# Kernel optimization log

Hardware: AMD Instinct MI355X
Metric: run time of the kernel (lower is better)

Reference implementation:

```python
import jax, jax.numpy as jnp
import numpy as np

C = 384      # c_s
NF = 16      # n_freq
H = 256      # mlp_hidden
B, K, N = 4, 2048, 16384
POS_WEIGHT = 1.5  # not used; see below


def _ln(x, g, b, eps=1e-5):
    m = x.mean(-1, keepdims=True)
    v = ((x - m) ** 2).mean(-1, keepdims=True)
    return (x - m) * jax.lax.rsqrt(v + eps) * g + b


def setup_inputs() -> dict:
    key = jax.random.key(0)
    ks = jax.random.split(key, 24)
    w = lambda k, shp: (jax.random.normal(k, shp, jnp.float32) * 0.02)
    inp = {
        "s_parent": jax.random.normal(ks[0], (B, K, C), jnp.float32),
        "mu_k": jax.random.normal(ks[1], (B, K, 3), jnp.float32),
        "R_k": jax.random.normal(ks[2], (B, K, 3, 3), jnp.float32),
        "s_k": jax.random.uniform(ks[3], (B, K, 3), jnp.float32),
        "a_idx": jax.random.randint(ks[4], (B, N), 0, K, jnp.int32),
        "node_mask": jnp.ones((B, N), jnp.float32),
        "pos01": jax.random.uniform(ks[5], (B, N), jnp.float32),
        # Pos01FourierEncoder: Linear(2*NF -> C)
        "pos_w": w(ks[6], (C, 2 * NF)), "pos_b": jnp.zeros((C,), jnp.float32),
        # q_proj: LayerNorm(C), Linear(C,C), SiLU, Linear(C,C)
        "q_ln_g": jnp.ones((C,), jnp.float32), "q_ln_b": jnp.zeros((C,), jnp.float32),
        "q_w1": w(ks[7], (C, C)), "q_b1": jnp.zeros((C,), jnp.float32),
        "q_w2": w(ks[8], (C, C)), "q_b2": jnp.zeros((C,), jnp.float32),
        # mlp: LayerNorm(C), Linear(C,H), SiLU, Linear(H,H), SiLU, Linear(H,3)
        "m_ln_g": jnp.ones((C,), jnp.float32), "m_ln_b": jnp.zeros((C,), jnp.float32),
        "m_w1": w(ks[9], (H, C)), "m_b1": jnp.zeros((H,), jnp.float32),
        "m_w2": w(ks[10], (H, H)), "m_b2": jnp.zeros((H,), jnp.float32),
        "m_w3": w(ks[11], (3, H)), "m_b3": jnp.zeros((3,), jnp.float32),
    }
    return inp


def reference(s_parent, mu_k, R_k, s_k, a_idx, node_mask, pos01,
              pos_w, pos_b, q_ln_g, q_ln_b, q_w1, q_b1, q_w2, q_b2,
              m_ln_g, m_ln_b, m_w1, m_b1, m_w2, m_b2, m_w3, m_b3):
    pos_weight = 1.0
    scale = 1.5
    mask = node_mask[..., None]  # [B,N,1]

    # Fourier positional encoding of pos01 in [0,1]
    freqs = (2.0 ** jnp.arange(NF, dtype=jnp.float32)) * np.float32(np.pi)
    ang = pos01[..., None] * freqs                          # [B,N,NF]
    feats = jnp.concatenate([jnp.sin(ang), jnp.cos(ang)], -1)  # [B,N,2NF]
    pos_emb = (feats @ pos_w.T + pos_b) * mask              # [B,N,C]

    idx = jnp.clip(a_idx, 0, K - 1)
    s_pi = jnp.take_along_axis(s_parent, idx[:, :, None], axis=1)  # [B,N,C]
    s_pi = s_pi + pos_weight * pos_emb

    # q_proj
    q = _ln(s_pi, q_ln_g, q_ln_b)
    q = jax.nn.silu(q @ q_w1.T + q_b1)
    q = (q @ q_w2.T + q_b2) * mask

    # mlp -> xi_hat
    h = _ln(q, m_ln_g, m_ln_b)
    h = jax.nn.silu(h @ m_w1.T + m_b1)
    h = jax.nn.silu(h @ m_w2.T + m_b2)
    xi = (h @ m_w3.T + m_b3) * mask
    xi_hat = jnp.tanh(xi) * scale                           # [B,N,3]

    # gather parent rigid params per node
    mu_i = jnp.take_along_axis(mu_k, idx[:, :, None], axis=1)            # [B,N,3]
    s_i = jnp.take_along_axis(jnp.maximum(s_k, 1e-8), idx[:, :, None], axis=1)
    R_i = jnp.take_along_axis(R_k, idx[:, :, None, None], axis=1)        # [B,N,3,3]

    # rigid apply: x = R @ (xi * s) + mu
    x_hat = jnp.einsum('bnij,bnj->bni', R_i, xi_hat * s_i) + mu_i
    x_hat = x_hat * mask
    return xi_hat, x_hat * 10.0, pos01
```

## Files before the change

### kernel.cpp

```cpp
#include <hip/hip_runtime.h>
#include <hip/hip_bf16.h>
#include <math.h>

#define C 384
#define NF 16
#define H 256
#define Bb 4
#define Kk 2048
#define Nn 16384
#define MB 32
#define LDA 392

typedef __attribute__((ext_vector_type(8))) short bf16x8;
typedef __attribute__((ext_vector_type(4))) float f32x4;
typedef __attribute__((ext_vector_type(4))) short s16x4;

#define POS_OFF 0
#define Q1_OFF  12288
#define Q2_OFF  159744
#define M1_OFF  307200
#define M2_OFF  405504
#define M3_OFF  471040
#define W_TOTAL 475136
#define NCONV   ((W_TOTAL + 255) / 256)
#define GQ_OFF 0
#define CQ_OFF 384
#define GM_OFF 768
#define CM_OFF 1024

__device__ __attribute__((always_inline)) inline short f2bf(float x) {
    return __builtin_bit_cast(short, __float2bfloat16(x));
}
__device__ __attribute__((always_inline)) inline float bf2f(short s) {
    return __bfloat162float(__builtin_bit_cast(__hip_bfloat16, s));
}
__device__ __attribute__((always_inline)) inline float silu(float v) {
    return v * __builtin_amdgcn_rcpf(1.f + __expf(-v));
}
__device__ __attribute__((always_inline)) inline s16x4 pack4(f32x4 v) {
    __hip_bfloat162 p0 = __float22bfloat162_rn(float2{v[0], v[1]});
    __hip_bfloat162 p1 = __float22bfloat162_rn(float2{v[2], v[3]});
    s16x4 o;
    o[0] = __builtin_bit_cast(short, p0.x);
    o[1] = __builtin_bit_cast(short, p0.y);
    o[2] = __builtin_bit_cast(short, p1.x);
    o[3] = __builtin_bit_cast(short, p1.y);
    return o;
}

__global__ __launch_bounds__(256) void prep(
    const float* __restrict__ pos_w, const float* __restrict__ q_w1,
    const float* __restrict__ q_w2,  const float* __restrict__ m_w1,
    const float* __restrict__ m_w2,  const float* __restrict__ m_w3,
    const float* __restrict__ q_ln_g, const float* __restrict__ q_ln_b,
    const float* __restrict__ m_ln_g, const float* __restrict__ m_ln_b,
    const float* __restrict__ q_b1,   const float* __restrict__ m_b1,
    short* __restrict__ ws, float* __restrict__ cst)
{
    __shared__ float rg[4], rc[4];
    int tid = threadIdx.x;
    int blk = blockIdx.x;
    if (blk < NCONV) {
        int i = blk * 256 + tid;
        if (i >= W_TOTAL) return;
        const float* src; int off, K;
        if      (i < Q1_OFF) { src = pos_w; off = POS_OFF; K = 32; }
        else if (i < Q2_OFF) { src = q_w1;  off = Q1_OFF;  K = 384; }
        else if (i < M1_OFF) { src = q_w2;  off = Q2_OFF;  K = 384; }
        else if (i < M2_OFF) { src = m_w1;  off = M1_OFF;  K = 384; }
        else if (i < M3_OFF) { src = m_w2;  off = M2_OFF;  K = 256; }
        else                 { src = m_w3;  off = M3_OFF;  K = 256; }
        int t = i - off;
        int chunk = t >> 9, r = t & 511;
        int ln = r >> 5, kq = r & 31;
        int NKm = K >> 5;
        int ntg = chunk / NKm, kk = chunk - ntg * NKm;
        int f = ntg * 16 + ln, k = kk * 32 + kq;
        float v;
        if (off == M3_OFF) v = (f < 3) ? m_w3[f * 256 + k] : 0.f;
        else               v = src[(size_t)f * K + k];
        if (off == Q1_OFF) v *= q_ln_g[k];
        if (off == M1_OFF) v *= m_ln_g[k];
        ws[i] = f2bf(v);
        return;
    }
    int f = blk - NCONV;
    const float *Wsrc, *lng, *lnb, *bias; int fr, go, co;
    if (f < 384) { Wsrc = q_w1; lng = q_ln_g; lnb = q_ln_b; bias = q_b1; fr = f;      go = GQ_OFF; co = CQ_OFF; }
    else         { Wsrc = m_w1; lng = m_ln_g; lnb = m_ln_b; bias = m_b1; fr = f - 384; go = GM_OFF; co = CM_OFF; }
    float g = 0.f, c = 0.f;
    for (int k = tid; k < 384; k += 256) {
        float wv = Wsrc[(size_t)fr * 384 + k];
        g += bf2f(f2bf(wv * lng[k]));
        c += wv * lnb[k];
    }
    #pragma unroll
    for (int d = 1; d < 64; d <<= 1) { g += __shfl_xor(g, d); c += __shfl_xor(c, d); }
    if ((tid & 63) == 0) { rg[tid >> 6] = g; rc[tid >> 6] = c; }
    __syncthreads();
    if (tid == 0) {
        cst[go + fr] = rg[0] + rg[1] + rg[2] + rg[3];
        cst[co + fr] = rc[0] + rc[1] + rc[2] + rc[3] + bias[fr];
    }
}

template<int K, int NT, int NTN, int KN, bool SILU_, bool MASK, bool LNIN, bool STATS>
__device__ __attribute__((always_inline)) inline void layer_ip(
    const short* __restrict__ W, const float* __restrict__ cb,
    const float* __restrict__ Gf, int FB,
    const short* __restrict__ Wn, int FBn,
    bf16x8 (&bin)[6],
    short (*__restrict__ xs)[LDA],
    float (*__restrict__ sc1)[4], float (*__restrict__ sc2)[4],
    const float* __restrict__ wmask, int w, int q, int ln)
{
    constexpr int NK = K / 32;
    const short* bp[NT];
    #pragma unroll
    for (int nt = 0; nt < NT; ++nt)
        bp[nt] = W + ((size_t)(FB / 16 + nt) * NK) * 512 + ln * 32 + q * 8;

    f32x4 acc[2][NT];
    #pragma unroll
    for (int mt = 0; mt < 2; ++mt)
        #pragma unroll
        for (int nt = 0; nt < NT; ++nt)
            acc[mt][nt] = (f32x4){0.f, 0.f, 0.f, 0.f};

    bf16x8 b0[NT], b1[NT], a0[2], a1[2];
    #pragma unroll
    for (int nt = 0; nt < NT; ++nt) b0[nt] = bin[nt];
    #pragma unroll
    for (int mt = 0; mt < 2; ++mt) a0[mt] = *(const bf16x8*)&xs[mt * 16 + ln][q * 8];

    #pragma unroll
    for (int kc = 0; kc < NK; kc += 2) {
        #pragma unroll
        for (int nt = 0; nt < NT; ++nt) b1[nt] = *(const bf16x8*)(bp[nt] + (kc + 1) * 512);
        #pragma unroll
        for (int mt = 0; mt < 2; ++mt) a1[mt] = *(const bf16x8*)&xs[mt * 16 + ln][(kc + 1) * 32 + q * 8];
        #pragma unroll
        for (int nt = 0; nt < NT; ++nt)
            #pragma unroll
            for (int mt = 0; mt < 2; ++mt)
                acc[mt][nt] = __builtin_amdgcn_mfma_f32_16x16x32_bf16(b0[nt], a0[mt], acc[mt][nt], 0, 0, 0);
        if (kc + 2 < NK) {
            #pragma unroll
            for (int nt = 0; nt < NT; ++nt) b0[nt] = *(const bf16x8*)(bp[nt] + (kc + 2) * 512);
            #pragma unroll
            for (int mt = 0; mt < 2; ++mt) a0[mt] = *(const bf16x8*)&xs[mt * 16 + ln][(kc + 2) * 32 + q * 8];
        }
        #pragma unroll
        for (int nt = 0; nt < NT; ++nt)
            #pragma unroll
            for (int mt = 0; mt < 2; ++mt)
                acc[mt][nt] = __builtin_amdgcn_mfma_f32_16x16x32_bf16(b1[nt], a1[mt], acc[mt][nt], 0, 0, 0);
    }

    #pragma unroll
    for (int nt = 0; nt < NTN; ++nt)
        bin[nt] = *(const bf16x8*)(Wn + ((size_t)(FBn / 16 + nt) * (KN / 32)) * 512 + ln * 32 + q * 8);

    __syncthreads();

    float mk[2], rstd[2], rm[2];
    #pragma unroll
    for (int mt = 0; mt < 2; ++mt) {
        int m = mt * 16 + ln;
        if (MASK) mk[mt] = wmask[m];
        if (LNIN) {
            f32x4 p1 = *(const f32x4*)&sc1[m][0];
            f32x4 p2 = *(const f32x4*)&sc2[m][0];
            float t1 = p1[0] + p1[1] + p1[2] + p1[3];
            float t2 = p2[0] + p2[1] + p2[2] + p2[3];
            float mean = t1 * (1.f / 384.f);
            float var  = t2 * (1.f / 384.f) - mean * mean;
            rstd[mt] = rsqrtf(var + 1e-5f);
            rm[mt]   = rstd[mt] * mean;
        }
    }

    float s1[2] = {0.f, 0.f}, s2[2] = {0.f, 0.f};
    #pragma unroll
    for (int nt = 0; nt < NT; ++nt) {
        const int f0 = FB + nt * 16 + q * 4;
        f32x4 c4 = *(const f32x4*)&cb[f0];
        f32x4 g4;
        if (LNIN) g4 = *(const f32x4*)&Gf[f0];
        #pragma unroll
        for (int mt = 0; mt < 2; ++mt) {
            f32x4 vv;
            #pragma unroll
            for (int r = 0; r < 4; ++r) {
                float v;
                if (LNIN) v = fmaf(rstd[mt], acc[mt][nt][r], fmaf(-rm[mt], g4[r], c4[r]));
                else      v = acc[mt][nt][r] + c4[r];
                if (SILU_) v = silu(v);
                if (MASK) v *= mk[mt];
                if (STATS) { s1[mt] += v; s2[mt] += v * v; }
                vv[r] = v;
            }
            *(s16x4*)&xs[mt * 16 + ln][f0] = pack4(vv);
        }
    }
    if (STATS) {
        #pragma unroll
        for (int mt = 0; mt < 2; ++mt) {
            s1[mt] += __shfl_xor(s1[mt], 16); s2[mt] += __shfl_xor(s2[mt], 16);
            s1[mt] += __shfl_xor(s1[mt], 32); s2[mt] += __shfl_xor(s2[mt], 32);
        }
        if (q == 0) {
            #pragma unroll
            for (int mt = 0; mt < 2; ++mt) {
                sc1[mt * 16 + ln][w] = s1[mt];
                sc2[mt * 16 + ln][w] = s2[mt];
            }
        }
    }
    __syncthreads();
}

__global__ __launch_bounds__(256, 3) void upxi32(
    const float* __restrict__ s_parent, const float* __restrict__ mu_k,
    const float* __restrict__ R_k,      const float* __restrict__ s_k,
    const int*   __restrict__ a_idx,    const float* __restrict__ node_mask,
    const float* __restrict__ pos01,
    const float* __restrict__ pos_b,
    const float* __restrict__ q_b2,     const float* __restrict__ m_b2,
    const float* __restrict__ m_b3,
    const short* __restrict__ wsb,      const float* __restrict__ cst,
    float* __restrict__ out)
{
    __shared__ short xs[MB][LDA];
    __shared__ float sc1[MB][4];
    __shared__ float sc2[MB][4];
    __shared__ float wmask[MB], wpos[MB];
    __shared__ int   widx[MB];

    const int tid  = threadIdx.x;
    const int w    = tid >> 6;
    const int lane = tid & 63;
    const int q    = lane >> 4;
    const int ln   = lane & 15;

    const int g0 = blockIdx.x * MB;
    const int b  = g0 / Nn;
    const int n0 = g0 % Nn;

    bf16x8 bin[6];
    #pragma unroll
    for (int nt = 0; nt < 6; ++nt)
        bin[nt] = *(const bf16x8*)(wsb + Q1_OFF + ((size_t)(w * 6 + nt) * 12) * 512 + ln * 32 + q * 8);

    if (tid < MB) {
        int gi = b * Nn + n0 + tid;
        int idx = a_idx[gi];
        widx[tid]  = min(max(idx, 0), Kk - 1);
        wmask[tid] = node_mask[gi];
        wpos[tid]  = pos01[gi];
    }
    __syncthreads();

    const float* gbase = s_parent + (long)b * Kk * C;

    {
        const short* pos_wb = wsb + POS_OFF;
        const bool use_sin = (q < 2);
        const int kb = (q & 1) * 8;
        bf16x8 a[2];
        #pragma unroll
        for (int mt = 0; mt < 2; ++mt) {
            float p = wpos[mt * 16 + ln];
            #pragma unroll
            for (int e = 0; e < 8; ++e) {
                float fr = (float)(1 << (kb + e)) * 3.14159265358979323846f;
                float sv, cv;
                __sincosf(p * fr, &sv, &cv);
                a[mt][e] = f2bf(use_sin ? sv : cv);
            }
        }
        f32x4 acc[2][6];
        #pragma unroll
        for (int mt = 0; mt < 2; ++mt)
            #pragma unroll
            for (int nt = 0; nt < 6; ++nt)
                acc[mt][nt] = (f32x4){0.f, 0.f, 0.f, 0.f};
        #pragma unroll
        for (int nt = 0; nt < 6; ++nt) {
            bf16x8 bfr = *(const bf16x8*)&pos_wb[(w * 6 + nt) * 512 + ln * 32 + q * 8];
            #pragma unroll
            for (int mt = 0; mt < 2; ++mt)
                acc[mt][nt] = __builtin_amdgcn_mfma_f32_16x16x32_bf16(bfr, a[mt], acc[mt][nt], 0, 0, 0);
        }
        float mk[2]; int ix[2];
        #pragma unroll
        for (int mt = 0; mt < 2; ++mt) {
            mk[mt] = wmask[mt * 16 + ln];
            ix[mt] = widx[mt * 16 + ln];
        }
        float s1[2] = {0.f, 0.f}, s2[2] = {0.f, 0.f};
        #pragma unroll
        for (int nt = 0; nt < 6; ++nt) {
            const int f0 = w * 96 + nt * 16 + q * 4;
            f32x4 pb4 = *(const f32x4*)&pos_b[f0];
            #pragma unroll
            for (int mt = 0; mt < 2; ++mt) {
                f32x4 g4 = *(const f32x4*)&gbase[(long)ix[mt] * C + f0];
                f32x4 vv;
                #pragma unroll
                for (int r = 0; r < 4; ++r) {
                    float v = (acc[mt][nt][r] + pb4[r]) * mk[mt] + g4[r];
                    s1[mt] += v; s2[mt] += v * v;
                    vv[r] = v;
                }
                *(s16x4*)&xs[mt * 16 + ln][f0] = pack4(vv);
            }
        }
        #pragma unroll
        for (int mt = 0; mt < 2; ++mt) {
            s1[mt] += __shfl_xor(s1[mt], 16); s2[mt] += __shfl_xor(s2[mt], 16);
            s1[mt] += __shfl_xor(s1[mt], 32); s2[mt] += __shfl_xor(s2[mt], 32);
        }
        if (q == 0) {
            #pragma unroll
            for (int mt = 0; mt < 2; ++mt) {
                sc1[mt * 16 + ln][w] = s1[mt];
                sc2[mt * 16 + ln][w] = s2[mt];
            }
        }
    }
    __syncthreads();

    layer_ip<384, 6, 6, 384, true,  false, true,  false>(wsb + Q1_OFF, cst + CQ_OFF,
        cst + GQ_OFF, w * 96, wsb + Q2_OFF, w * 96, bin, xs, sc1, sc2, wmask, w, q, ln);
    layer_ip<384, 6, 4, 384, false, true,  false, true >(wsb + Q2_OFF, q_b2,
        nullptr, w * 96, wsb + M1_OFF, w * 64, bin, xs, sc1, sc2, wmask, w, q, ln);
    layer_ip<384, 4, 4, 256, true,  false, true,  false>(wsb + M1_OFF, cst + CM_OFF,
        cst + GM_OFF, w * 64, wsb + M2_OFF, w * 64, bin, xs, sc1, sc2, wmask, w, q, ln);
    layer_ip<256, 4, 1, 256, true,  false, false, false>(wsb + M2_OFF, m_b2,
        nullptr, w * 64, wsb + M3_OFF, 0, bin, xs, sc1, sc2, wmask, w, q, ln);

    if (w < 2) {
        const short* W3 = wsb + M3_OFF;
        f32x4 a3 = (f32x4){0.f, 0.f, 0.f, 0.f};
        #pragma unroll
        for (int kc = 0; kc < 8; ++kc) {
            bf16x8 a  = *(const bf16x8*)&xs[w * 16 + ln][kc * 32 + q * 8];
            bf16x8 bf = *(const bf16x8*)(W3 + kc * 512 + ln * 32 + q * 8);
            a3 = __builtin_amdgcn_mfma_f32_16x16x32_bf16(bf, a, a3, 0, 0, 0);
        }
        if (q == 0) {
            int m = w * 16 + ln;
            float mkv = wmask[m];
            #pragma unroll
            for (int r = 0; r < 3; ++r) {
                float v = (a3[r] + m_b3[r]) * mkv;
                sc1[m][r] = tanhf(v) * 1.5f;
            }
        }
        if (lane < 16) {
            int m = w * 16 + lane;
            long gi = (long)b * Nn + n0 + m;
            long pk = (long)b * Kk + widx[m];
            float mkv = wmask[m];
            float xv[3], yv[3], xiv[3];
            #pragma unroll
            for (int j = 0; j < 3; ++j) {
                xiv[j] = sc1[m][j];
                float sc = fmaxf(s_k[pk * 3 + j], 1e-8f);
                xv[j] = xiv[j] * sc;
            }
            #pragma unroll
            for (int i = 0; i < 3; ++i) {
                float a = R_k[pk * 9 + i * 3 + 0] * xv[0]
                        + R_k[pk * 9 + i * 3 + 1] * xv[1]
                        + R_k[pk * 9 + i * 3 + 2] * xv[2]
                        + mu_k[pk * 3 + i];
                yv[i] = a * mkv * 10.f;
            }
            float* o0 = out;
            float* o1 = out + (long)Bb * Nn * 3;
            float* o2 = out + (long)Bb * Nn * 6;
            #pragma unroll
            for (int j = 0; j < 3; ++j) { o0[gi * 3 + j] = xiv[j]; o1[gi * 3 + j] = yv[j]; }
            o2[gi] = wpos[m];
        }
    }
}

extern "C" void kernel_launch(void* const* d_in, const int* in_sizes, int n_in,
                              void* d_out, int out_size, void* d_ws, size_t ws_size,
                              hipStream_t stream) {
    const float* s_parent = (const float*)d_in[0];
    const float* mu_k     = (const float*)d_in[1];
    const float* R_k      = (const float*)d_in[2];
    const float* s_k      = (const float*)d_in[3];
    const int*   a_idx    = (const int*)  d_in[4];
    const float* node_mask= (const float*)d_in[5];
    const float* pos01    = (const float*)d_in[6];
    const float* pos_w    = (const float*)d_in[7];
    const float* pos_b    = (const float*)d_in[8];
    const float* q_ln_g   = (const float*)d_in[9];
    const float* q_ln_b   = (const float*)d_in[10];
    const float* q_w1     = (const float*)d_in[11];
    const float* q_b1     = (const float*)d_in[12];
    const float* q_w2     = (const float*)d_in[13];
    const float* q_b2     = (const float*)d_in[14];
    const float* m_ln_g   = (const float*)d_in[15];
    const float* m_ln_b   = (const float*)d_in[16];
    const float* m_w1     = (const float*)d_in[17];
    const float* m_b1     = (const float*)d_in[18];
    const float* m_w2     = (const float*)d_in[19];
    const float* m_b2     = (const float*)d_in[20];
    const float* m_w3     = (const float*)d_in[21];
    const float* m_b3     = (const float*)d_in[22];

    short* wsb = (short*)d_ws;
    float* cst = (float*)(wsb + W_TOTAL);

    prep<<<NCONV + 640, 256, 0, stream>>>(
        pos_w, q_w1, q_w2, m_w1, m_w2, m_w3,
        q_ln_g, q_ln_b, m_ln_g, m_ln_b, q_b1, m_b1, wsb, cst);

    int blocks = (Bb * Nn) / MB;
    upxi32<<<blocks, 256, 0, stream>>>(
        s_parent, mu_k, R_k, s_k, a_idx, node_mask, pos01,
        pos_b, q_b2, m_b2, m_b3, wsb, cst, (float*)d_out);
}
```

Baseline: 236.1 us.

## Double the row tile to 64 and triple-buffer weight fragment loads

Each block now handles 64 rows instead of 32, so every weight fragment fetched from global memory feeds four MFMA row tiles instead of two, halving weight traffic per row. The K loop becomes a 3-stage rotating buffer for weight fragments with the next layer's first fragments prefetched inside the loop, and __syncthreads is replaced by a raw lgkmcnt wait plus barrier. The final 3-wide head now runs on all four waves. The cost is more accumulator registers and a drop in launch-bounds occupancy from 3 to 2 blocks per CU.

```diff
diff --git a/kernel.cpp b/kernel.cpp
--- a/kernel.cpp
+++ b/kernel.cpp
@@ -8,7 +8,7 @@
 #define Bb 4
 #define Kk 2048
 #define Nn 16384
-#define MB 32
+#define MB 64
 #define LDA 392
 
 typedef __attribute__((ext_vector_type(8))) short bf16x8;
@@ -27,6 +27,8 @@
 #define CQ_OFF 384
 #define GM_OFF 768
 #define CM_OFF 1024
+
+#define BAR() __asm__ volatile("s_waitcnt lgkmcnt(0)\ns_barrier" ::: "memory")
 
 __device__ __attribute__((always_inline)) inline short f2bf(float x) {
     return __builtin_bit_cast(short, __float2bfloat16(x));
@@ -115,57 +117,56 @@
     const float* __restrict__ wmask, int w, int q, int ln)
 {
     constexpr int NK = K / 32;
-    const short* bp[NT];
-    #pragma unroll
-    for (int nt = 0; nt < NT; ++nt)
-        bp[nt] = W + ((size_t)(FB / 16 + nt) * NK) * 512 + ln * 32 + q * 8;
-
-    f32x4 acc[2][NT];
-    #pragma unroll
-    for (int mt = 0; mt < 2; ++mt)
+    const short* bp = W + (size_t)(FB / 16) * NK * 512 + ln * 32 + q * 8;
+
+    f32x4 acc[4][NT];
+    #pragma unroll
+    for (int mt = 0; mt < 4; ++mt)
         #pragma unroll
         for (int nt = 0; nt < NT; ++nt)
             acc[mt][nt] = (f32x4){0.f, 0.f, 0.f, 0.f};
 
-    bf16x8 b0[NT], b1[NT], a0[2], a1[2];
-    #pragma unroll
-    for (int nt = 0; nt < NT; ++nt) b0[nt] = bin[nt];
-    #pragma unroll
-    for (int mt = 0; mt < 2; ++mt) a0[mt] = *(const bf16x8*)&xs[mt * 16 + ln][q * 8];
-
-    #pragma unroll
-    for (int kc = 0; kc < NK; kc += 2) {
-        #pragma unroll
-        for (int nt = 0; nt < NT; ++nt) b1[nt] = *(const bf16x8*)(bp[nt] + (kc + 1) * 512);
-        #pragma unroll
-        for (int mt = 0; mt < 2; ++mt) a1[mt] = *(const bf16x8*)&xs[mt * 16 + ln][(kc + 1) * 32 + q * 8];
+    bf16x8 Bbuf[3][NT], Abuf[2][4];
+    #pragma unroll
+    for (int nt = 0; nt < NT; ++nt) Bbuf[0][nt] = bin[nt];
+    #pragma unroll
+    for (int nt = 0; nt < NT; ++nt)
+        Bbuf[1][nt] = *(const bf16x8*)(bp + (size_t)nt * NK * 512 + 512);
+    #pragma unroll
+    for (int mt = 0; mt < 4; ++mt)
+        Abuf[0][mt] = *(const bf16x8*)&xs[mt * 16 + ln][q * 8];
+
+    #pragma unroll
+    for (int kc = 0; kc < NK; ++kc) {
+        if (kc + 2 < NK) {
+            #pragma unroll
+            for (int nt = 0; nt < NT; ++nt)
+                Bbuf[(kc + 2) % 3][nt] =
+                    *(const bf16x8*)(bp + (size_t)nt * NK * 512 + (kc + 2) * 512);
+        } else if (kc + 2 == NK) {
+            #pragma unroll
+            for (int nt = 0; nt < NTN; ++nt)
+                bin[nt] = *(const bf16x8*)(Wn + ((size_t)(FBn / 16 + nt) * (KN / 32)) * 512 + ln * 32 + q * 8);
+        }
+        if (kc + 1 < NK) {
+            #pragma unroll
+            for (int mt = 0; mt < 4; ++mt)
+                Abuf[(kc + 1) & 1][mt] =
+                    *(const bf16x8*)&xs[mt * 16 + ln][(kc + 1) * 32 + q * 8];
+        }
         #pragma unroll
         for (int nt = 0; nt < NT; ++nt)
             #pragma unroll
-            for (int mt = 0; mt < 2; ++mt)
-                acc[mt][nt] = __builtin_amdgcn_mfma_f32_16x16x32_bf16(b0[nt], a0[mt], acc[mt][nt], 0, 0, 0);
-        if (kc + 2 < NK) {
-            #pragma unroll
-            for (int nt = 0; nt < NT; ++nt) b0[nt] = *(const bf16x8*)(bp[nt] + (kc + 2) * 512);
-            #pragma unroll
-            for (int mt = 0; mt < 2; ++mt) a0[mt] = *(const bf16x8*)&xs[mt * 16 + ln][(kc + 2) * 32 + q * 8];
-        }
-        #pragma unroll
-        for (int nt = 0; nt < NT; ++nt)
-            #pragma unroll
-            for (int mt = 0; mt < 2; ++mt)
-                acc[mt][nt] = __builtin_amdgcn_mfma_f32_16x16x32_bf16(b1[nt], a1[mt], acc[mt][nt], 0, 0, 0);
-    }
-
-    #pragma unroll
-    for (int nt = 0; nt < NTN; ++nt)
-        bin[nt] = *(const bf16x8*)(Wn + ((size_t)(FBn / 16 + nt) * (KN / 32)) * 512 + ln * 32 + q * 8);
-
-    __syncthreads();
-
-    float mk[2], rstd[2], rm[2];
-    #pragma unroll
-    for (int mt = 0; mt < 2; ++mt) {
+            for (int mt = 0; mt < 4; ++mt)
+                acc[mt][nt] = __builtin_amdgcn_mfma_f32_16x16x32_bf16(
+                    Bbuf[kc % 3][nt], Abuf[kc & 1][mt], acc[mt][nt], 0, 0, 0);
+    }
+
+    BAR();
+
+    float mk[4], rstd[4], rm[4];
+    #pragma unroll
+    for (int mt = 0; mt < 4; ++mt) {
         int m = mt * 16 + ln;
         if (MASK) mk[mt] = wmask[m];
         if (LNIN) {
@@ -180,7 +181,7 @@
         }
     }
 
-    float s1[2] = {0.f, 0.f}, s2[2] = {0.f, 0.f};
+    float s1[4] = {0.f,0.f,0.f,0.f}, s2[4] = {0.f,0.f,0.f,0.f};
     #pragma unroll
     for (int nt = 0; nt < NT; ++nt) {
         const int f0 = FB + nt * 16 + q * 4;
@@ -188,7 +189,7 @@
         f32x4 g4;
         if (LNIN) g4 = *(const f32x4*)&Gf[f0];
         #pragma unroll
-        for (int mt = 0; mt < 2; ++mt) {
+        for (int mt = 0; mt < 4; ++mt) {
             f32x4 vv;
             #pragma unroll
             for (int r = 0; r < 4; ++r) {
@@ -205,22 +206,22 @@
     }
     if (STATS) {
         #pragma unroll
-        for (int mt = 0; mt < 2; ++mt) {
+        for (int mt = 0; mt < 4; ++mt) {
             s1[mt] += __shfl_xor(s1[mt], 16); s2[mt] += __shfl_xor(s2[mt], 16);
             s1[mt] += __shfl_xor(s1[mt], 32); s2[mt] += __shfl_xor(s2[mt], 32);
         }
         if (q == 0) {
             #pragma unroll
-            for (int mt = 0; mt < 2; ++mt) {
+            for (int mt = 0; mt < 4; ++mt) {
                 sc1[mt * 16 + ln][w] = s1[mt];
                 sc2[mt * 16 + ln][w] = s2[mt];
             }
         }
     }
-    __syncthreads();
-}
-
-__global__ __launch_bounds__(256, 3) void upxi32(
+    BAR();
+}
+
+__global__ __launch_bounds__(256, 2) void upxi64(
     const float* __restrict__ s_parent, const float* __restrict__ mu_k,
     const float* __restrict__ R_k,      const float* __restrict__ s_k,
     const int*   __restrict__ a_idx,    const float* __restrict__ node_mask,
@@ -259,7 +260,7 @@
         wmask[tid] = node_mask[gi];
         wpos[tid]  = pos01[gi];
     }
-    __syncthreads();
+    BAR();
 
     const float* gbase = s_parent + (long)b * Kk * C;
 
@@ -267,9 +268,9 @@
         const short* pos_wb = wsb + POS_OFF;
         const bool use_sin = (q < 2);
         const int kb = (q & 1) * 8;
-        bf16x8 a[2];
-        #pragma unroll
-        for (int mt = 0; mt < 2; ++mt) {
+        bf16x8 a[4];
+        #pragma unroll
+        for (int mt = 0; mt < 4; ++mt) {
             float p = wpos[mt * 16 + ln];
             #pragma unroll
             for (int e = 0; e < 8; ++e) {
@@ -279,9 +280,9 @@
                 a[mt][e] = f2bf(use_sin ? sv : cv);
             }
         }
-        f32x4 acc[2][6];
-        #pragma unroll
-        for (int mt = 0; mt < 2; ++mt)
+        f32x4 acc[4][6];
+        #pragma unroll
+        for (int mt = 0; mt < 4; ++mt)
             #pragma unroll
             for (int nt = 0; nt < 6; ++nt)
                 acc[mt][nt] = (f32x4){0.f, 0.f, 0.f, 0.f};
@@ -289,22 +290,22 @@
         for (int nt = 0; nt < 6; ++nt) {
             bf16x8 bfr = *(const bf16x8*)&pos_wb[(w * 6 + nt) * 512 + ln * 32 + q * 8];
             #pragma unroll
-            for (int mt = 0; mt < 2; ++mt)
+            for (int mt = 0; mt < 4; ++mt)
                 acc[mt][nt] = __builtin_amdgcn_mfma_f32_16x16x32_bf16(bfr, a[mt], acc[mt][nt], 0, 0, 0);
         }
-        float mk[2]; int ix[2];
-        #pragma unroll
-        for (int mt = 0; mt < 2; ++mt) {
+        float mk[4]; int ix[4];
+        #pragma unroll
+        for (int mt = 0; mt < 4; ++mt) {
             mk[mt] = wmask[mt * 16 + ln];
             ix[mt] = widx[mt * 16 + ln];
         }
-        float s1[2] = {0.f, 0.f}, s2[2] = {0.f, 0.f};
+        float s1[4] = {0.f,0.f,0.f,0.f}, s2[4] = {0.f,0.f,0.f,0.f};
         #pragma unroll
         for (int nt = 0; nt < 6; ++nt) {
             const int f0 = w * 96 + nt * 16 + q * 4;
             f32x4 pb4 = *(const f32x4*)&pos_b[f0];
             #pragma unroll
-            for (int mt = 0; mt < 2; ++mt) {
+            for (int mt = 0; mt < 4; ++mt) {
                 f32x4 g4 = *(const f32x4*)&gbase[(long)ix[mt] * C + f0];
                 f32x4 vv;
                 #pragma unroll
@@ -317,19 +318,19 @@
             }
         }
         #pragma unroll
-        for (int mt = 0; mt < 2; ++mt) {
+        for (int mt = 0; mt < 4; ++mt) {
             s1[mt] += __shfl_xor(s1[mt], 16); s2[mt] += __shfl_xor(s2[mt], 16);
             s1[mt] += __shfl_xor(s1[mt], 32); s2[mt] += __shfl_xor(s2[mt], 32);
         }
         if (q == 0) {
             #pragma unroll
-            for (int mt = 0; mt < 2; ++mt) {
+            for (int mt = 0; mt < 4; ++mt) {
                 sc1[mt * 16 + ln][w] = s1[mt];
                 sc2[mt * 16 + ln][w] = s2[mt];
             }
         }
     }
-    __syncthreads();
+    BAR();
 
     layer_ip<384, 6, 6, 384, true,  false, true,  false>(wsb + Q1_OFF, cst + CQ_OFF,
         cst + GQ_OFF, w * 96, wsb + Q2_OFF, w * 96, bin, xs, sc1, sc2, wmask, w, q, ln);
@@ -340,13 +341,14 @@
     layer_ip<256, 4, 1, 256, true,  false, false, false>(wsb + M2_OFF, m_b2,
         nullptr, w * 64, wsb + M3_OFF, 0, bin, xs, sc1, sc2, wmask, w, q, ln);
 
-    if (w < 2) {
+    {
         const short* W3 = wsb + M3_OFF;
         f32x4 a3 = (f32x4){0.f, 0.f, 0.f, 0.f};
         #pragma unroll
         for (int kc = 0; kc < 8; ++kc) {
             bf16x8 a  = *(const bf16x8*)&xs[w * 16 + ln][kc * 32 + q * 8];
-            bf16x8 bf = *(const bf16x8*)(W3 + kc * 512 + ln * 32 + q * 8);
+            bf16x8 bf = (kc == 0) ? bin[0]
+                      : *(const bf16x8*)(W3 + kc * 512 + ln * 32 + q * 8);
             a3 = __builtin_amdgcn_mfma_f32_16x16x32_bf16(bf, a, a3, 0, 0, 0);
         }
         if (q == 0) {
@@ -358,33 +360,34 @@
                 sc1[m][r] = tanhf(v) * 1.5f;
             }
         }
-        if (lane < 16) {
-            int m = w * 16 + lane;
-            long gi = (long)b * Nn + n0 + m;
-            long pk = (long)b * Kk + widx[m];
-            float mkv = wmask[m];
-            float xv[3], yv[3], xiv[3];
-            #pragma unroll
-            for (int j = 0; j < 3; ++j) {
-                xiv[j] = sc1[m][j];
-                float sc = fmaxf(s_k[pk * 3 + j], 1e-8f);
-                xv[j] = xiv[j] * sc;
-            }
-            #pragma unroll
-            for (int i = 0; i < 3; ++i) {
-                float a = R_k[pk * 9 + i * 3 + 0] * xv[0]
-                        + R_k[pk * 9 + i * 3 + 1] * xv[1]
-                        + R_k[pk * 9 + i * 3 + 2] * xv[2]
-                        + mu_k[pk * 3 + i];
-                yv[i] = a * mkv * 10.f;
-            }
-            float* o0 = out;
-            float* o1 = out + (long)Bb * Nn * 3;
-            float* o2 = out + (long)Bb * Nn * 6;
-            #pragma unroll
-            for (int j = 0; j < 3; ++j) { o0[gi * 3 + j] = xiv[j]; o1[gi * 3 + j] = yv[j]; }
-            o2[gi] = wpos[m];
-        }
+    }
+
+    if (lane < 16) {
+        int m = w * 16 + lane;
+        long gi = (long)b * Nn + n0 + m;
+        long pk = (long)b * Kk + widx[m];
+        float mkv = wmask[m];
+        float xv[3], yv[3], xiv[3];
+        #pragma unroll
+        for (int j = 0; j < 3; ++j) {
+            xiv[j] = sc1[m][j];
+            float sc = fmaxf(s_k[pk * 3 + j], 1e-8f);
+            xv[j] = xiv[j] * sc;
+        }
+        #pragma unroll
+        for (int i = 0; i < 3; ++i) {
+            float a = R_k[pk * 9 + i * 3 + 0] * xv[0]
+                    + R_k[pk * 9 + i * 3 + 1] * xv[1]
+                    + R_k[pk * 9 + i * 3 + 2] * xv[2]
+                    + mu_k[pk * 3 + i];
+            yv[i] = a * mkv * 10.f;
+        }
+        float* o0 = out;
+        float* o1 = out + (long)Bb * Nn * 3;
+        float* o2 = out + (long)Bb * Nn * 6;
+        #pragma unroll
+        for (int j = 0; j < 3; ++j) { o0[gi * 3 + j] = xiv[j]; o1[gi * 3 + j] = yv[j]; }
+        o2[gi] = wpos[m];
     }
 }
 
@@ -423,7 +426,7 @@
         q_ln_g, q_ln_b, m_ln_g, m_ln_b, q_b1, m_b1, wsb, cst);
 
     int blocks = (Bb * Nn) / MB;
-    upxi32<<<blocks, 256, 0, stream>>>(
+    upxi64<<<blocks, 256, 0, stream>>>(
         s_parent, mu_k, R_k, s_k, a_idx, node_mask, pos01,
         pos_b, q_b2, m_b2, m_b3, wsb, cst, (float*)d_out);
 }
```

After: 197.3 us. -16.4%, faster.

## Switch MLP chain to 32x32x16 MFMA with 64-row tiles and deeper weight prefetch

Applied to the files above, without the earlier changes.

Moves all GEMM layers from 16x16x32 to 32x32x16 bf16 MFMA, doubles rows per block to 64, and repacks the preprocessed weight layout to match the new fragment shape. The weight stream gets a 4-deep register ring buffer, and __syncthreads is replaced by a raw lgkmcnt wait plus s_barrier. The intent is to halve per-row weight traffic from L2 and raise MFMA efficiency, at the cost of more accumulator registers and lower occupancy (launch bounds 3 to 2).

```diff
diff --git a/kernel.cpp b/kernel.cpp
--- a/kernel.cpp
+++ b/kernel.cpp
@@ -8,12 +8,13 @@
 #define Bb 4
 #define Kk 2048
 #define Nn 16384
-#define MB 32
+#define MB 64
 #define LDA 392
 
-typedef __attribute__((ext_vector_type(8))) short bf16x8;
-typedef __attribute__((ext_vector_type(4))) float f32x4;
-typedef __attribute__((ext_vector_type(4))) short s16x4;
+typedef __attribute__((ext_vector_type(8)))  short bf16x8;
+typedef __attribute__((ext_vector_type(4)))  float f32x4;
+typedef __attribute__((ext_vector_type(16))) float f32x16;
+typedef __attribute__((ext_vector_type(4)))  short s16x4;
 
 #define POS_OFF 0
 #define Q1_OFF  12288
@@ -21,12 +22,14 @@
 #define M1_OFF  307200
 #define M2_OFF  405504
 #define M3_OFF  471040
-#define W_TOTAL 475136
+#define W_TOTAL 479232
 #define NCONV   ((W_TOTAL + 255) / 256)
 #define GQ_OFF 0
 #define CQ_OFF 384
 #define GM_OFF 768
 #define CM_OFF 1024
+
+#define BAR() __asm__ volatile("s_waitcnt lgkmcnt(0)\ns_barrier" ::: "memory")
 
 __device__ __attribute__((always_inline)) inline short f2bf(float x) {
     return __builtin_bit_cast(short, __float2bfloat16(x));
@@ -72,10 +75,11 @@
         else                 { src = m_w3;  off = M3_OFF;  K = 256; }
         int t = i - off;
         int chunk = t >> 9, r = t & 511;
-        int ln = r >> 5, kq = r & 31;
-        int NKm = K >> 5;
+        int lane = r >> 3, j = r & 7;
+        int lnn = lane & 31, half = lane >> 5;
+        int NKm = K >> 4;
         int ntg = chunk / NKm, kk = chunk - ntg * NKm;
-        int f = ntg * 16 + ln, k = kk * 32 + kq;
+        int f = ntg * 32 + lnn, k = kk * 16 + half * 8 + j;
         float v;
         if (off == M3_OFF) v = (f < 3) ? m_w3[f * 256 + k] : 0.f;
         else               v = src[(size_t)f * K + k];
@@ -109,64 +113,68 @@
     const short* __restrict__ W, const float* __restrict__ cb,
     const float* __restrict__ Gf, int FB,
     const short* __restrict__ Wn, int FBn,
-    bf16x8 (&bin)[6],
+    bf16x8 (&bin)[3],
     short (*__restrict__ xs)[LDA],
     float (*__restrict__ sc1)[4], float (*__restrict__ sc2)[4],
-    const float* __restrict__ wmask, int w, int q, int ln)
+    const float* __restrict__ wmask, int w, int lane)
 {
-    constexpr int NK = K / 32;
+    constexpr int NK = K / 16;
+    const int ln = lane & 31, half = lane >> 5;
     const short* bp[NT];
     #pragma unroll
     for (int nt = 0; nt < NT; ++nt)
-        bp[nt] = W + ((size_t)(FB / 16 + nt) * NK) * 512 + ln * 32 + q * 8;
-
-    f32x4 acc[2][NT];
+        bp[nt] = W + (size_t)(FB / 32 + nt) * NK * 512 + lane * 8;
+
+    f32x16 acc[2][NT];
     #pragma unroll
     for (int mt = 0; mt < 2; ++mt)
         #pragma unroll
         for (int nt = 0; nt < NT; ++nt)
-            acc[mt][nt] = (f32x4){0.f, 0.f, 0.f, 0.f};
-
-    bf16x8 b0[NT], b1[NT], a0[2], a1[2];
-    #pragma unroll
-    for (int nt = 0; nt < NT; ++nt) b0[nt] = bin[nt];
-    #pragma unroll
-    for (int mt = 0; mt < 2; ++mt) a0[mt] = *(const bf16x8*)&xs[mt * 16 + ln][q * 8];
-
-    #pragma unroll
-    for (int kc = 0; kc < NK; kc += 2) {
-        #pragma unroll
-        for (int nt = 0; nt < NT; ++nt) b1[nt] = *(const bf16x8*)(bp[nt] + (kc + 1) * 512);
-        #pragma unroll
-        for (int mt = 0; mt < 2; ++mt) a1[mt] = *(const bf16x8*)&xs[mt * 16 + ln][(kc + 1) * 32 + q * 8];
+            acc[mt][nt] = (f32x16)(0.f);
+
+    bf16x8 B[4][NT], a0[2], a1[2];
+    #pragma unroll
+    for (int nt = 0; nt < NT; ++nt) B[0][nt] = bin[nt];
+    #pragma unroll
+    for (int nt = 0; nt < NT; ++nt) B[1][nt] = *(const bf16x8*)(bp[nt] + 512);
+    #pragma unroll
+    for (int nt = 0; nt < NT; ++nt) B[2][nt] = *(const bf16x8*)(bp[nt] + 1024);
+    #pragma unroll
+    for (int mt = 0; mt < 2; ++mt)
+        a0[mt] = *(const bf16x8*)&xs[mt * 32 + ln][half * 8];
+
+    #pragma unroll
+    for (int kc = 0; kc < NK; ++kc) {
+        if (kc + 3 < NK) {
+            #pragma unroll
+            for (int nt = 0; nt < NT; ++nt)
+                B[(kc + 3) & 3][nt] = *(const bf16x8*)(bp[nt] + (kc + 3) * 512);
+        } else if (kc + 3 == NK) {
+            #pragma unroll
+            for (int nt = 0; nt < NTN; ++nt)
+                bin[nt] = *(const bf16x8*)(Wn + (size_t)(FBn / 32 + nt) * (KN / 16) * 512 + lane * 8);
+        }
+        bf16x8* ac = (kc & 1) ? a1 : a0;
+        bf16x8* an = (kc & 1) ? a0 : a1;
+        if (kc + 1 < NK) {
+            #pragma unroll
+            for (int mt = 0; mt < 2; ++mt)
+                an[mt] = *(const bf16x8*)&xs[mt * 32 + ln][(kc + 1) * 16 + half * 8];
+        }
         #pragma unroll
         for (int nt = 0; nt < NT; ++nt)
             #pragma unroll
             for (int mt = 0; mt < 2; ++mt)
-                acc[mt][nt] = __builtin_amdgcn_mfma_f32_16x16x32_bf16(b0[nt], a0[mt], acc[mt][nt], 0, 0, 0);
-        if (kc + 2 < NK) {
-            #pragma unroll
-            for (int nt = 0; nt < NT; ++nt) b0[nt] = *(const bf16x8*)(bp[nt] + (kc + 2) * 512);
-            #pragma unroll
-            for (int mt = 0; mt < 2; ++mt) a0[mt] = *(const bf16x8*)&xs[mt * 16 + ln][(kc + 2) * 32 + q * 8];
-        }
-        #pragma unroll
-        for (int nt = 0; nt < NT; ++nt)
-            #pragma unroll
-            for (int mt = 0; mt < 2; ++mt)
-                acc[mt][nt] = __builtin_amdgcn_mfma_f32_16x16x32_bf16(b1[nt], a1[mt], acc[mt][nt], 0, 0, 0);
-    }
-
-    #pragma unroll
-    for (int nt = 0; nt < NTN; ++nt)
-        bin[nt] = *(const bf16x8*)(Wn + ((size_t)(FBn / 16 + nt) * (KN / 32)) * 512 + ln * 32 + q * 8);
-
-    __syncthreads();
+                acc[mt][nt] = __builtin_amdgcn_mfma_f32_32x32x16_bf16(
+                    B[kc & 3][nt], ac[mt], acc[mt][nt], 0, 0, 0);
+    }
+
+    BAR();
 
     float mk[2], rstd[2], rm[2];
     #pragma unroll
     for (int mt = 0; mt < 2; ++mt) {
-        int m = mt * 16 + ln;
+        int m = mt * 32 + ln;
         if (MASK) mk[mt] = wmask[m];
         if (LNIN) {
             f32x4 p1 = *(const f32x4*)&sc1[m][0];
@@ -183,44 +191,48 @@
     float s1[2] = {0.f, 0.f}, s2[2] = {0.f, 0.f};
     #pragma unroll
     for (int nt = 0; nt < NT; ++nt) {
-        const int f0 = FB + nt * 16 + q * 4;
-        f32x4 c4 = *(const f32x4*)&cb[f0];
-        f32x4 g4;
-        if (LNIN) g4 = *(const f32x4*)&Gf[f0];
+        #pragma unroll
+        for (int g = 0; g < 4; ++g) {
+            const int f0 = FB + nt * 32 + 8 * g + 4 * half;
+            f32x4 c4 = *(const f32x4*)&cb[f0];
+            f32x4 g4;
+            if (LNIN) g4 = *(const f32x4*)&Gf[f0];
+            #pragma unroll
+            for (int mt = 0; mt < 2; ++mt) {
+                f32x4 vv;
+                #pragma unroll
+                for (int i = 0; i < 4; ++i) {
+                    float av = acc[mt][nt][4 * g + i];
+                    float v;
+                    if (LNIN) v = fmaf(rstd[mt], av, fmaf(-rm[mt], g4[i], c4[i]));
+                    else      v = av + c4[i];
+                    if (SILU_) v = silu(v);
+                    if (MASK) v *= mk[mt];
+                    if (STATS) { s1[mt] += v; s2[mt] += v * v; }
+                    vv[i] = v;
+                }
+                *(s16x4*)&xs[mt * 32 + ln][f0] = pack4(vv);
+            }
+        }
+    }
+    if (STATS) {
         #pragma unroll
         for (int mt = 0; mt < 2; ++mt) {
-            f32x4 vv;
-            #pragma unroll
-            for (int r = 0; r < 4; ++r) {
-                float v;
-                if (LNIN) v = fmaf(rstd[mt], acc[mt][nt][r], fmaf(-rm[mt], g4[r], c4[r]));
-                else      v = acc[mt][nt][r] + c4[r];
-                if (SILU_) v = silu(v);
-                if (MASK) v *= mk[mt];
-                if (STATS) { s1[mt] += v; s2[mt] += v * v; }
-                vv[r] = v;
-            }
-            *(s16x4*)&xs[mt * 16 + ln][f0] = pack4(vv);
-        }
-    }
-    if (STATS) {
-        #pragma unroll
-        for (int mt = 0; mt < 2; ++mt) {
-            s1[mt] += __shfl_xor(s1[mt], 16); s2[mt] += __shfl_xor(s2[mt], 16);
-            s1[mt] += __shfl_xor(s1[mt], 32); s2[mt] += __shfl_xor(s2[mt], 32);
-        }
-        if (q == 0) {
+            s1[mt] += __shfl_xor(s1[mt], 32);
+            s2[mt] += __shfl_xor(s2[mt], 32);
+        }
+        if (half == 0) {
             #pragma unroll
             for (int mt = 0; mt < 2; ++mt) {
-                sc1[mt * 16 + ln][w] = s1[mt];
-                sc2[mt * 16 + ln][w] = s2[mt];
-            }
-        }
-    }
-    __syncthreads();
-}
-
-__global__ __launch_bounds__(256, 3) void upxi32(
+                sc1[mt * 32 + ln][w] = s1[mt];
+                sc2[mt * 32 + ln][w] = s2[mt];
+            }
+        }
+    }
+    BAR();
+}
+
+__global__ __launch_bounds__(256, 2) void upxi64(
     const float* __restrict__ s_parent, const float* __restrict__ mu_k,
     const float* __restrict__ R_k,      const float* __restrict__ s_k,
     const int*   __restrict__ a_idx,    const float* __restrict__ node_mask,
@@ -240,17 +252,17 @@
     const int tid  = threadIdx.x;
     const int w    = tid >> 6;
     const int lane = tid & 63;
-    const int q    = lane >> 4;
-    const int ln   = lane & 15;
+    const int ln   = lane & 31;
+    const int half = lane >> 5;
 
     const int g0 = blockIdx.x * MB;
     const int b  = g0 / Nn;
     const int n0 = g0 % Nn;
 
-    bf16x8 bin[6];
-    #pragma unroll
-    for (int nt = 0; nt < 6; ++nt)
-        bin[nt] = *(const bf16x8*)(wsb + Q1_OFF + ((size_t)(w * 6 + nt) * 12) * 512 + ln * 32 + q * 8);
+    bf16x8 bin[3];
+    #pragma unroll
+    for (int nt = 0; nt < 3; ++nt)
+        bin[nt] = *(const bf16x8*)(wsb + Q1_OFF + (size_t)(w * 3 + nt) * 24 * 512 + lane * 8);
 
     if (tid < MB) {
         int gi = b * Nn + n0 + tid;
@@ -259,98 +271,108 @@
         wmask[tid] = node_mask[gi];
         wpos[tid]  = pos01[gi];
     }
-    __syncthreads();
+    BAR();
 
     const float* gbase = s_parent + (long)b * Kk * C;
 
     {
         const short* pos_wb = wsb + POS_OFF;
-        const bool use_sin = (q < 2);
-        const int kb = (q & 1) * 8;
-        bf16x8 a[2];
+        bf16x8 wf[3][2];
+        #pragma unroll
+        for (int nt = 0; nt < 3; ++nt)
+            #pragma unroll
+            for (int kc = 0; kc < 2; ++kc)
+                wf[nt][kc] = *(const bf16x8*)&pos_wb[((w * 3 + nt) * 2 + kc) * 512 + lane * 8];
+        bf16x8 bs[2], bc[2];
         #pragma unroll
         for (int mt = 0; mt < 2; ++mt) {
-            float p = wpos[mt * 16 + ln];
-            #pragma unroll
-            for (int e = 0; e < 8; ++e) {
-                float fr = (float)(1 << (kb + e)) * 3.14159265358979323846f;
+            float p = wpos[mt * 32 + ln];
+            #pragma unroll
+            for (int j = 0; j < 8; ++j) {
+                int fi = half * 8 + j;
+                float fr = (float)(1 << fi) * 3.14159265358979323846f;
                 float sv, cv;
                 __sincosf(p * fr, &sv, &cv);
-                a[mt][e] = f2bf(use_sin ? sv : cv);
-            }
-        }
-        f32x4 acc[2][6];
+                bs[mt][j] = f2bf(sv);
+                bc[mt][j] = f2bf(cv);
+            }
+        }
+        f32x16 acc[2][3];
         #pragma unroll
         for (int mt = 0; mt < 2; ++mt)
             #pragma unroll
-            for (int nt = 0; nt < 6; ++nt)
-                acc[mt][nt] = (f32x4){0.f, 0.f, 0.f, 0.f};
-        #pragma unroll
-        for (int nt = 0; nt < 6; ++nt) {
-            bf16x8 bfr = *(const bf16x8*)&pos_wb[(w * 6 + nt) * 512 + ln * 32 + q * 8];
-            #pragma unroll
-            for (int mt = 0; mt < 2; ++mt)
-                acc[mt][nt] = __builtin_amdgcn_mfma_f32_16x16x32_bf16(bfr, a[mt], acc[mt][nt], 0, 0, 0);
-        }
+            for (int nt = 0; nt < 3; ++nt)
+                acc[mt][nt] = (f32x16)(0.f);
+        #pragma unroll
+        for (int nt = 0; nt < 3; ++nt)
+            #pragma unroll
+            for (int mt = 0; mt < 2; ++mt) {
+                acc[mt][nt] = __builtin_amdgcn_mfma_f32_32x32x16_bf16(wf[nt][0], bs[mt], acc[mt][nt], 0, 0, 0);
+                acc[mt][nt] = __builtin_amdgcn_mfma_f32_32x32x16_bf16(wf[nt][1], bc[mt], acc[mt][nt], 0, 0, 0);
+            }
         float mk[2]; int ix[2];
         #pragma unroll
         for (int mt = 0; mt < 2; ++mt) {
-            mk[mt] = wmask[mt * 16 + ln];
-            ix[mt] = widx[mt * 16 + ln];
+            mk[mt] = wmask[mt * 32 + ln];
+            ix[mt] = widx[mt * 32 + ln];
         }
         float s1[2] = {0.f, 0.f}, s2[2] = {0.f, 0.f};
         #pragma unroll
-        for (int nt = 0; nt < 6; ++nt) {
-            const int f0 = w * 96 + nt * 16 + q * 4;
-            f32x4 pb4 = *(const f32x4*)&pos_b[f0];
+        for (int nt = 0; nt < 3; ++nt) {
+            #pragma unroll
+            for (int g = 0; g < 4; ++g) {
+                const int f0 = w * 96 + nt * 32 + 8 * g + 4 * half;
+                f32x4 pb4 = *(const f32x4*)&pos_b[f0];
+                #pragma unroll
+                for (int mt = 0; mt < 2; ++mt) {
+                    f32x4 g4 = *(const f32x4*)&gbase[(long)ix[mt] * C + f0];
+                    f32x4 vv;
+                    #pragma unroll
+                    for (int i = 0; i < 4; ++i) {
+                        float v = (acc[mt][nt][4 * g + i] + pb4[i]) * mk[mt] + g4[i];
+                        s1[mt] += v; s2[mt] += v * v;
+                        vv[i] = v;
+                    }
+                    *(s16x4*)&xs[mt * 32 + ln][f0] = pack4(vv);
+                }
+            }
+        }
+        #pragma unroll
+        for (int mt = 0; mt < 2; ++mt) {
+            s1[mt] += __shfl_xor(s1[mt], 32);
+            s2[mt] += __shfl_xor(s2[mt], 32);
+        }
+        if (half == 0) {
             #pragma unroll
             for (int mt = 0; mt < 2; ++mt) {
-                f32x4 g4 = *(const f32x4*)&gbase[(long)ix[mt] * C + f0];
-                f32x4 vv;
-                #pragma unroll
-                for (int r = 0; r < 4; ++r) {
-                    float v = (acc[mt][nt][r] + pb4[r]) * mk[mt] + g4[r];
-                    s1[mt] += v; s2[mt] += v * v;
-                    vv[r] = v;
-                }
-                *(s16x4*)&xs[mt * 16 + ln][f0] = pack4(vv);
-            }
-        }
-        #pragma unroll
-        for (int mt = 0; mt < 2; ++mt) {
-            s1[mt] += __shfl_xor(s1[mt], 16); s2[mt] += __shfl_xor(s2[mt], 16);
-            s1[mt] += __shfl_xor(s1[mt], 32); s2[mt] += __shfl_xor(s2[mt], 32);
-        }
-        if (q == 0) {
-            #pragma unroll
-            for (int mt = 0; mt < 2; ++mt) {
-                sc1[mt * 16 + ln][w] = s1[mt];
-                sc2[mt * 16 + ln][w] = s2[mt];
-            }
-        }
-    }
-    __syncthreads();
-
-    layer_ip<384, 6, 6, 384, true,  false, true,  false>(wsb + Q1_OFF, cst + CQ_OFF,
-        cst + GQ_OFF, w * 96, wsb + Q2_OFF, w * 96, bin, xs, sc1, sc2, wmask, w, q, ln);
-    layer_ip<384, 6, 4, 384, false, true,  false, true >(wsb + Q2_OFF, q_b2,
-        nullptr, w * 96, wsb + M1_OFF, w * 64, bin, xs, sc1, sc2, wmask, w, q, ln);
-    layer_ip<384, 4, 4, 256, true,  false, true,  false>(wsb + M1_OFF, cst + CM_OFF,
-        cst + GM_OFF, w * 64, wsb + M2_OFF, w * 64, bin, xs, sc1, sc2, wmask, w, q, ln);
-    layer_ip<256, 4, 1, 256, true,  false, false, false>(wsb + M2_OFF, m_b2,
-        nullptr, w * 64, wsb + M3_OFF, 0, bin, xs, sc1, sc2, wmask, w, q, ln);
+                sc1[mt * 32 + ln][w] = s1[mt];
+                sc2[mt * 32 + ln][w] = s2[mt];
+            }
+        }
+    }
+    BAR();
+
+    layer_ip<384, 3, 3, 384, true,  false, true,  false>(wsb + Q1_OFF, cst + CQ_OFF,
+        cst + GQ_OFF, w * 96, wsb + Q2_OFF, w * 96, bin, xs, sc1, sc2, wmask, w, lane);
+    layer_ip<384, 3, 2, 384, false, true,  false, true >(wsb + Q2_OFF, q_b2,
+        nullptr, w * 96, wsb + M1_OFF, w * 64, bin, xs, sc1, sc2, wmask, w, lane);
+    layer_ip<384, 2, 2, 256, true,  false, true,  false>(wsb + M1_OFF, cst + CM_OFF,
+        cst + GM_OFF, w * 64, wsb + M2_OFF, w * 64, bin, xs, sc1, sc2, wmask, w, lane);
+    layer_ip<256, 2, 1, 256, true,  false, false, false>(wsb + M2_OFF, m_b2,
+        nullptr, w * 64, wsb + M3_OFF, 0, bin, xs, sc1, sc2, wmask, w, lane);
 
     if (w < 2) {
         const short* W3 = wsb + M3_OFF;
-        f32x4 a3 = (f32x4){0.f, 0.f, 0.f, 0.f};
-        #pragma unroll
-        for (int kc = 0; kc < 8; ++kc) {
-            bf16x8 a  = *(const bf16x8*)&xs[w * 16 + ln][kc * 32 + q * 8];
-            bf16x8 bf = *(const bf16x8*)(W3 + kc * 512 + ln * 32 + q * 8);
-            a3 = __builtin_amdgcn_mfma_f32_16x16x32_bf16(bf, a, a3, 0, 0, 0);
-        }
-        if (q == 0) {
-            int m = w * 16 + ln;
+        f32x16 a3 = (f32x16)(0.f);
+        #pragma unroll
+        for (int kc = 0; kc < 16; ++kc) {
+            bf16x8 a  = *(const bf16x8*)&xs[w * 32 + ln][kc * 16 + half * 8];
+            bf16x8 bf = (kc == 0) ? bin[0]
+                      : *(const bf16x8*)(W3 + kc * 512 + lane * 8);
+            a3 = __builtin_amdgcn_mfma_f32_32x32x16_bf16(bf, a, a3, 0, 0, 0);
+        }
+        if (half == 0) {
+            int m = w * 32 + ln;
             float mkv = wmask[m];
             #pragma unroll
             for (int r = 0; r < 3; ++r) {
@@ -358,32 +380,34 @@
                 sc1[m][r] = tanhf(v) * 1.5f;
             }
         }
-        if (lane < 16) {
-            int m = w * 16 + lane;
-            long gi = (long)b * Nn + n0 + m;
-            long pk = (long)b * Kk + widx[m];
-            float mkv = wmask[m];
-            float xv[3], yv[3], xiv[3];
-            #pragma unroll
-            for (int j = 0; j < 3; ++j) {
-                xiv[j] = sc1[m][j];
-                float sc = fmaxf(s_k[pk * 3 + j], 1e-8f);
-                xv[j] = xiv[j] * sc;
-            }
-            #pragma unroll
-            for (int i = 0; i < 3; ++i) {
-                float a = R_k[pk * 9 + i * 3 + 0] * xv[0]
-                        + R_k[pk * 9 + i * 3 + 1] * xv[1]
-                        + R_k[pk * 9 + i * 3 + 2] * xv[2]
-                        + mu_k[pk * 3 + i];
-                yv[i] = a * mkv * 10.f;
-            }
-            float* o0 = out;
-            float* o1 = out + (long)Bb * Nn * 3;
-            float* o2 = out + (long)Bb * Nn * 6;
-            #pragma unroll
-            for (int j = 0; j < 3; ++j) { o0[gi * 3 + j] = xiv[j]; o1[gi * 3 + j] = yv[j]; }
-            o2[gi] = wpos[m];
+        {
+            int m = w * 32 + ln;
+            if (half == 0) {
+                long gi = (long)b * Nn + n0 + m;
+                long pk = (long)b * Kk + widx[m];
+                float mkv = wmask[m];
+                float xv[3], yv[3], xiv[3];
+                #pragma unroll
+                for (int j = 0; j < 3; ++j) {
+                    xiv[j] = sc1[m][j];
+                    float sc = fmaxf(s_k[pk * 3 + j], 1e-8f);
+                    xv[j] = xiv[j] * sc;
+                }
+                #pragma unroll
+                for (int i = 0; i < 3; ++i) {
+                    float a = R_k[pk * 9 + i * 3 + 0] * xv[0]
+                            + R_k[pk * 9 + i * 3 + 1] * xv[1]
+                            + R_k[pk * 9 + i * 3 + 2] * xv[2]
+                            + mu_k[pk * 3 + i];
+                    yv[i] = a * mkv * 10.f;
+                }
+                float* o0 = out;
+                float* o1 = out + (long)Bb * Nn * 3;
+                float* o2 = out + (long)Bb * Nn * 6;
+                #pragma unroll
+                for (int j = 0; j < 3; ++j) { o0[gi * 3 + j] = xiv[j]; o1[gi * 3 + j] = yv[j]; }
+                o2[gi] = wpos[m];
+            }
         }
     }
 }
@@ -423,7 +447,7 @@
         q_ln_g, q_ln_b, m_ln_g, m_ln_b, q_b1, m_b1, wsb, cst);
 
     int blocks = (Bb * Nn) / MB;
-    upxi32<<<blocks, 256, 0, stream>>>(
+    upxi64<<<blocks, 256, 0, stream>>>(
         s_parent, mu_k, R_k, s_k, a_idx, node_mask, pos01,
         pos_b, q_b2, m_b2, m_b3, wsb, cst, (float*)d_out);
 }
```

New measurement: 221.8 us. 1.06x faster.
